# Kernel tuning notes

Hardware: AMD Instinct MI355X
Metric: run time of the kernel (lower is better)

The kernel has to match this reference:

```python
import jax, jax.numpy as jnp
import numpy as np

B, S, D = 64, 14, 2048   # batch, enc_image_size, encoder_dim
A, H, E = 512, 512, 512  # attention_dim, lstm_size, embedding_size
V, L = 10000, 20         # vocab_size, max caption length (T = L-1 decode steps)


def setup_inputs() -> dict:
    key = jax.random.key(0)
    ks = jax.random.split(key, 24)
    p = lambda k, shape: jax.random.normal(k, shape, jnp.float32) * 0.02
    features = jax.random.normal(ks[0], (B, S, S, D), jnp.float32)
    captions = jax.random.randint(ks[1], (B, L), 0, V)
    # sorted descending lengths in [2, L], max forced to L so T_dec = L-1
    lengths = jnp.sort(jax.random.randint(ks[2], (B,), 2, L + 1))[::-1]
    lengths = lengths.at[0].set(L)
    return {
        'features': features, 'captions': captions, 'lengths': lengths,
        'emb': p(ks[3], (V, E)),
        'W_ih': p(ks[4], (4 * H, D + E)), 'b_ih': p(ks[5], (4 * H,)),
        'W_hh': p(ks[6], (4 * H, H)), 'b_hh': p(ks[7], (4 * H,)),
        'h_fc_w': p(ks[8], (H, D)), 'h_fc_b': p(ks[9], (H,)),
        'c_fc_w': p(ks[10], (H, D)), 'c_fc_b': p(ks[11], (H,)),
        'f_beta_w': p(ks[12], (D, H)), 'f_beta_b': p(ks[13], (D,)),
        'cls_w': p(ks[14], (V, H)), 'cls_b': p(ks[15], (V,)),
        'enc_w': p(ks[16], (A, D)), 'enc_b': p(ks[17], (A,)),
        'dec_w': p(ks[18], (A, H)), 'dec_b': p(ks[19], (A,)),
        'att_w': p(ks[20], (1, A)), 'att_b': p(ks[21], (1,)),
    }


def reference(features, captions, lengths, emb, W_ih, b_ih, W_hh, b_hh,
              h_fc_w, h_fc_b, c_fc_w, c_fc_b, f_beta_w, f_beta_b,
              cls_w, cls_b, enc_w, enc_b, dec_w, dec_b, att_w, att_b):
    feats = features.reshape(features.shape[0], -1, features.shape[-1])  # (B,P,D)
    emb_seq = emb[captions]                                              # (B,L,E)
    mean_f = feats.mean(axis=1)
    h = mean_f @ h_fc_w.T + h_fc_b
    c = mean_f @ c_fc_w.T + c_fc_b
    dec_len = lengths - 1
    T = captions.shape[1] - 1
    # attention encoder projection is time-invariant: hoist out of the loop
    att1 = jnp.einsum('bpd,ad->bpa', feats, enc_w) + enc_b               # (B,P,A)

    def step(carry, xs):
        h, c = carry
        x_emb, t = xs
        att2 = h @ dec_w.T + dec_b                                       # (B,A)
        e = jnp.einsum('bpa,a->bp', jax.nn.relu(att1 + att2[:, None, :]), att_w[0]) + att_b[0]
        alpha = jax.nn.softmax(e, axis=1)                                # (B,P)
        awe = jnp.einsum('bp,bpd->bd', alpha, feats)
        gate = jax.nn.sigmoid(h @ f_beta_w.T + f_beta_b)
        awe = gate * awe
        x = jnp.concatenate([x_emb, awe], axis=1)                        # (B,E+D)
        gates = x @ W_ih.T + b_ih + h @ W_hh.T + b_hh                    # torch gate order i,f,g,o
        i, f, g, o = jnp.split(gates, 4, axis=1)
        c2 = jax.nn.sigmoid(f) * c + jax.nn.sigmoid(i) * jnp.tanh(g)
        h2 = jax.nn.sigmoid(o) * jnp.tanh(c2)
        y = h2 @ cls_w.T + cls_b                                         # dropout = eval identity
        active = (t < dec_len)[:, None]
        return (h2, c2), (jnp.where(active, y, 0.0), jnp.where(active, alpha, 0.0))

    xs = (jnp.swapaxes(emb_seq[:, :T], 0, 1), jnp.arange(T))
    (_, _), (y_pred, alphas) = jax.lax.scan(step, (h, c), xs)
    return jnp.swapaxes(y_pred, 0, 1), jnp.swapaxes(alphas, 0, 1)
```

## Files before the change

kernel.cpp:

```cpp
#include <hip/hip_runtime.h>
#include <math.h>

typedef __attribute__((ext_vector_type(8))) short bf16x8;
typedef __attribute__((ext_vector_type(8))) unsigned short u16x8;
typedef __attribute__((ext_vector_type(4))) float f32x4;

#define NB 64
#define NP 196
#define ND 2048
#define NA 512
#define NH 512
#define NE 512
#define NV 10000
#define NT 19
#define NROW (NB*NP)
#define NVP 10112
#define MROW 1280
#define PP 200

__device__ __forceinline__ unsigned short f2bu(float f){
    unsigned int u; __builtin_memcpy(&u, &f, 4);
    u = (u + 0x7FFFu + ((u >> 16) & 1u)) >> 16;
    return (unsigned short)u;
}
__device__ __forceinline__ float b2f(unsigned short s){
    unsigned int u = ((unsigned int)s) << 16;
    float f; __builtin_memcpy(&f, &u, 4); return f;
}
__device__ __forceinline__ float sigm(float x){ return 1.f/(1.f + __expf(-x)); }

__device__ __forceinline__ void gll16(const void* g, void* l){
    __builtin_amdgcn_global_load_lds(
        (const __attribute__((address_space(1))) void*)g,
        (__attribute__((address_space(3))) void*)l, 16, 0, 0);
}


__global__ void k_prep(const float4* __restrict__ enc_w, const float4* __restrict__ dec_w,
                       const float4* __restrict__ f_beta_w, const float4* __restrict__ W_ih,
                       const float4* __restrict__ W_hh, const float4* __restrict__ h_fc_w,
                       const float4* __restrict__ c_fc_w, const float4* __restrict__ cls_w,
                       ushort4* __restrict__ encwb, ushort4* __restrict__ whp,
                       ushort4* __restrict__ wgates, ushort4* __restrict__ wembb,
                       ushort4* __restrict__ whc, ushort4* __restrict__ clswb,
                       ushort4* __restrict__ hsb_pad){
    const int n0 = NA*ND/4;
    const int n1 = 2560*512/4;
    const int n2 = 2048*2560/4;
    const int n3 = 2048*512/4;
    const int n4 = 1024*2048/4;
    const int n5 = NVP*NH/4;
    const int n6 = 64*512/4;
    const int total = n0+n1+n2+n3+n4+n5+n6;
    int stride = gridDim.x*blockDim.x;
    for (int i = blockIdx.x*blockDim.x + threadIdx.x; i < total; i += stride){
        int idx = i;
        float4 v; ushort4 o;
        if (idx < n0){
            v = enc_w[idx];
            o.x = f2bu(v.x); o.y = f2bu(v.y); o.z = f2bu(v.z); o.w = f2bu(v.w);
            encwb[idx] = o; continue;
        }
        idx -= n0;
        if (idx < n1){
            v = (idx < 512*512/4) ? dec_w[idx] : f_beta_w[idx - 512*512/4];
            o.x = f2bu(v.x); o.y = f2bu(v.y); o.z = f2bu(v.z); o.w = f2bu(v.w);
            whp[idx] = o; continue;
        }
        idx -= n1;
        if (idx < n2){
            int j = idx / 640, kk4 = idx - j*640;
            v = (kk4 < 512) ? W_ih[(size_t)j*640 + 128 + kk4] : W_hh[(size_t)j*128 + (kk4 - 512)];
            o.x = f2bu(v.x); o.y = f2bu(v.y); o.z = f2bu(v.z); o.w = f2bu(v.w);
            wgates[idx] = o; continue;
        }
        idx -= n2;
        if (idx < n3){
            int j = idx >> 7, kk4 = idx & 127;
            v = W_ih[(size_t)j*640 + kk4];
            o.x = f2bu(v.x); o.y = f2bu(v.y); o.z = f2bu(v.z); o.w = f2bu(v.w);
            wembb[idx] = o; continue;
        }
        idx -= n3;
        if (idx < n4){
            v = (idx < 512*2048/4) ? h_fc_w[idx] : c_fc_w[idx - 512*2048/4];
            o.x = f2bu(v.x); o.y = f2bu(v.y); o.z = f2bu(v.z); o.w = f2bu(v.w);
            whc[idx] = o; continue;
        }
        idx -= n4;
        if (idx < n5){
            if (idx < NV*NH/4){
                v = cls_w[idx];
                o.x = f2bu(v.x); o.y = f2bu(v.y); o.z = f2bu(v.z); o.w = f2bu(v.w);
            } else { o.x = 0; o.y = 0; o.z = 0; o.w = 0; }
            clswb[idx] = o; continue;
        }
        idx -= n5;
        o.x = 0; o.y = 0; o.z = 0; o.w = 0;
        hsb_pad[idx] = o;
    }
}

__global__ void k_tr3(const float* __restrict__ feats,
                      unsigned short* __restrict__ fbf,
                      unsigned short* __restrict__ ftr,
                      float* __restrict__ mp){
    __shared__ unsigned short sm[64][260];
    __shared__ float4 msum[256];
    int dc = blockIdx.x;
    int b  = blockIdx.y;
    int ph = blockIdx.z;
    int tid = threadIdx.x;
    int c4 = tid & 63;
    int rq = tid >> 6;
    int D0 = dc*256;
    float4 acc = {0.f,0.f,0.f,0.f};
    for (int pcl = 0; pcl < 2; pcl++){
        int pc = ph*2 + pcl;
        __syncthreads();
        #pragma unroll
        for (int i = 0; i < 16; i++){
            int rl = rq + 4*i;
            int p = pc*64 + rl;
            float4 v = {0.f,0.f,0.f,0.f};
            if (p < NP) v = *(const float4*)(feats + ((size_t)(b*NP + p))*ND + D0 + c4*4);
            acc.x += v.x; acc.y += v.y; acc.z += v.z; acc.w += v.w;
            ushort4 u4;
            u4.x = f2bu(v.x); u4.y = f2bu(v.y); u4.z = f2bu(v.z); u4.w = f2bu(v.w);
            if (p < NP) *(ushort4*)(fbf + ((size_t)(b*NP + p))*ND + D0 + c4*4) = u4;
            *(ushort4*)&sm[rl][c4*4] = u4;
        }
        __syncthreads();
        int gmax = (pc == 3) ? 1 : 8;
        for (int g = 0; g < gmax; g++){
            u16x8 o;
            #pragma unroll
            for (int k = 0; k < 8; k++) o[k] = sm[g*8 + k][tid];
            *(u16x8*)(ftr + ((size_t)(b*ND + D0 + tid))*PP + pc*64 + g*8) = o;
        }
    }
    msum[tid] = acc;
    __syncthreads();
    if (tid < 64){
        float4 s0 = msum[tid], s1 = msum[tid+64], s2 = msum[tid+128], s3 = msum[tid+192];
        float4 tot = { (s0.x+s1.x)+(s2.x+s3.x), (s0.y+s1.y)+(s2.y+s3.y),
                       (s0.z+s1.z)+(s2.z+s3.z), (s0.w+s1.w)+(s2.w+s3.w) };
        *(float4*)(mp + ((size_t)ph*64 + b)*ND + D0 + tid*4) = tot;
    }
}

__global__ void k_mean2(const float* __restrict__ mp, unsigned short* __restrict__ meanbf){
    int i = blockIdx.x*1024 + threadIdx.x*4;
    float4 a = *(const float4*)(mp + i);
    float4 b = *(const float4*)(mp + 64*ND + i);
    ushort4 o;
    o.x = f2bu((a.x+b.x)*(1.f/196.f)); o.y = f2bu((a.y+b.y)*(1.f/196.f));
    o.z = f2bu((a.z+b.z)*(1.f/196.f)); o.w = f2bu((a.w+b.w)*(1.f/196.f));
    *(ushort4*)(meanbf + i) = o;
}

__global__ void k_embg(const float* __restrict__ emb, const int* __restrict__ captions,
                       unsigned short* __restrict__ embcat){
    int blk = blockIdx.x, tid = threadIdx.x;
    int r = blk*4 + (tid >> 6);
    int cg = tid & 63;
    u16x8 o;
    #pragma unroll
    for (int k = 0; k < 8; k++) o[k] = 0;
    if (r < NT*64){
        int t = r >> 6, b = r & 63;
        int tok = captions[b*20 + t];
        const float* e = emb + (size_t)tok*NE + cg*8;
        float4 v0 = *(const float4*)e;
        float4 v1 = *(const float4*)(e + 4);
        o[0] = f2bu(v0.x); o[1] = f2bu(v0.y); o[2] = f2bu(v0.z); o[3] = f2bu(v0.w);
        o[4] = f2bu(v1.x); o[5] = f2bu(v1.y); o[6] = f2bu(v1.z); o[7] = f2bu(v1.w);
    }
    *(u16x8*)(embcat + (size_t)r*NE + cg*8) = o;
}

__global__ void k_hc0m(const unsigned short* __restrict__ meanbf,
                       const unsigned short* __restrict__ whc,
                       const float* __restrict__ h_fc_b, const float* __restrict__ c_fc_b,
                       unsigned short* __restrict__ hbf, float* __restrict__ cst){
    int tid = threadIdx.x;
    int w = tid >> 6, l = tid & 63;
    int nt = blockIdx.x;
    int row = 16*w + (l & 15);
    int col = nt*16 + (l & 15);
    int kg = (l >> 4) * 8;
    f32x4 acc = {};
    for (int k0 = 0; k0 < ND; k0 += 32){
        bf16x8 af = *(const bf16x8*)(meanbf + (size_t)row*ND + k0 + kg);
        bf16x8 bv = *(const bf16x8*)(whc + (size_t)col*ND + k0 + kg);
        acc = __builtin_amdgcn_mfma_f32_16x16x32_bf16(af, bv, acc, 0, 0, 0);
    }
    int r0 = 16*w + (l >> 4)*4;
    #pragma unroll
    for (int r = 0; r < 4; r++){
        int b = r0 + r;
        if (col < 512) hbf[b*NH + col] = f2bu(acc[r] + h_fc_b[col]);
        else           cst[b*NH + (col - 512)] = acc[r] + c_fc_b[col - 512];
    }
}

template<int K>
__device__ __forceinline__ void gemm128(const unsigned short* __restrict__ A,
                                        const unsigned short* __restrict__ B,
                                        int brow, int bcol, f32x4 acc[4][4]){
    __shared__ unsigned short As[128*32];
    __shared__ unsigned short Bs[128*32];
    int tid = threadIdx.x;
    int w = tid >> 6, l = tid & 63;
    int wr = (w >> 1) * 64, wc = (w & 1) * 64;
    int lr = l & 15, kg = (l >> 4) * 8;
    const unsigned short* ga0 = A + (size_t)(brow + (tid >> 2))*K + (tid & 3)*8;
    const unsigned short* gb0 = B + (size_t)(bcol + (tid >> 2))*K + (tid & 3)*8;
    for (int k0 = 0; k0 < K; k0 += 32){
        __syncthreads();
        gll16(ga0 + k0,                As + w*512);
        gll16(ga0 + (size_t)64*K + k0, As + 2048 + w*512);
        gll16(gb0 + k0,                Bs + w*512);
        gll16(gb0 + (size_t)64*K + k0, Bs + 2048 + w*512);
        __syncthreads();
        bf16x8 af[4], bfr[4];
        #pragma unroll
        for (int mi = 0; mi < 4; mi++)
            af[mi] = *(const bf16x8*)(As + (wr + mi*16 + lr)*32 + kg);
        #pragma unroll
        for (int ni = 0; ni < 4; ni++)
            bfr[ni] = *(const bf16x8*)(Bs + (wc + ni*16 + lr)*32 + kg);
        #pragma unroll
        for (int ni = 0; ni < 4; ni++){
            #pragma unroll
            for (int mi = 0; mi < 4; mi++)
                acc[mi][ni] = __builtin_amdgcn_mfma_f32_16x16x32_bf16(af[mi], bfr[ni], acc[mi][ni], 0, 0, 0);
        }
    }
}

__global__ void k_gemm_att1(const unsigned short* __restrict__ fbf,
                            const unsigned short* __restrict__ encw,
                            const float* __restrict__ enc_b,
                            unsigned short* __restrict__ att1){
    f32x4 acc[4][4] = {};
    int brow = blockIdx.x*128, bcol = blockIdx.y*128;
    gemm128<ND>(fbf, encw, brow, bcol, acc);
    int w = threadIdx.x >> 6, l = threadIdx.x & 63;
    int wr = (w >> 1) * 64, wc = (w & 1) * 64;
    int r0 = brow + wr + (l >> 4)*4;
    int c0 = bcol + wc + (l & 15);
    #pragma unroll
    for (int ni = 0; ni < 4; ni++){
        int col = c0 + ni*16;
        float eb = enc_b[col];
        #pragma unroll
        for (int mi = 0; mi < 4; mi++){
            #pragma unroll
            for (int r = 0; r < 4; r++)
                att1[(size_t)(r0 + mi*16 + r)*NA + col] = f2bu(acc[mi][ni][r] + eb);
        }
    }
}

__global__ void k_gemb(const unsigned short* __restrict__ embcat,
                       const unsigned short* __restrict__ wembb,
                       const float* __restrict__ b_ih, const float* __restrict__ b_hh,
                       float* __restrict__ gemb){
    f32x4 acc[4][4] = {};
    int brow = blockIdx.x*128, bcol = blockIdx.y*128;
    gemm128<NE>(embcat, wembb, brow, bcol, acc);
    int w = threadIdx.x >> 6, l = threadIdx.x & 63;
    int wr = (w >> 1) * 64, wc = (w & 1) * 64;
    int r0 = brow + wr + (l >> 4)*4;
    int c0 = bcol + wc + (l & 15);
    #pragma unroll
    for (int ni = 0; ni < 4; ni++){
        int col = c0 + ni*16;
        float bias = b_ih[col] + b_hh[col];
        #pragma unroll
        for (int mi = 0; mi < 4; mi++){
            #pragma unroll
            for (int r = 0; r < 4; r++)
                gemb[(size_t)(r0 + mi*16 + r)*2048 + col] = acc[mi][ni][r] + bias;
        }
    }
}

__global__ void k_gemm_cls(const unsigned short* __restrict__ hsb,
                           const unsigned short* __restrict__ clsw,
                           const float* __restrict__ cls_b,
                           const int* __restrict__ lengths,
                           float* __restrict__ yout){
    f32x4 acc[4][4] = {};
    int brow = blockIdx.x*128, bcol = blockIdx.y*128;
    gemm128<NH>(hsb, clsw, brow, bcol, acc);
    int w = threadIdx.x >> 6, l = threadIdx.x & 63;
    int wr = (w >> 1) * 64, wc = (w & 1) * 64;
    int r0 = brow + wr + (l >> 4)*4;
    int c0 = bcol + wc + (l & 15);
    #pragma unroll
    for (int ni = 0; ni < 4; ni++){
        int col = c0 + ni*16;
        if (col >= NV) continue;
        float cb = cls_b[col];
        #pragma unroll
        for (int mi = 0; mi < 4; mi++){
            #pragma unroll
            for (int r = 0; r < 4; r++){
                int grow = r0 + mi*16 + r;
                if (grow >= NT*64) continue;
                int t = grow >> 6, bb = grow & 63;
                int active = t < (lengths[bb] - 1);
                yout[((size_t)bb*NT + t)*NV + col] = active ? (acc[mi][ni][r] + cb) : 0.f;
            }
        }
    }
}


__global__ void k_lstm(const float* __restrict__ part, const float* __restrict__ gemb,
                       float* __restrict__ cst, unsigned short* __restrict__ hbf,
                       unsigned short* __restrict__ hsb, int t){
    int idx = blockIdx.x*256 + threadIdx.x;
    int b = idx >> 9, j = idx & 511;
    const float* ge = gemb + ((size_t)(t - 1)*64 + b)*2048;
    float gi = ge[j], gf = ge[512 + j], gg = ge[1024 + j], go = ge[1536 + j];
    #pragma unroll
    for (int s = 0; s < 10; s++){
        const float* pb = part + (size_t)(s*64 + b)*2048;
        gi += pb[j]; gf += pb[512 + j]; gg += pb[1024 + j]; go += pb[1536 + j];
    }
    float c = cst[b*NH + j];
    float c2 = sigm(gf)*c + sigm(gi)*tanhf(gg);
    float h2 = sigm(go)*tanhf(c2);
    cst[b*NH + j] = c2;
    unsigned short u = f2bu(h2);
    hbf[b*NH + j] = u;
    hsb[((size_t)(t - 1)*64 + b)*NH + j] = u;
}

__global__ void k_hproj(const unsigned short* __restrict__ hbf,
                        const unsigned short* __restrict__ whp,
                        const float* __restrict__ dec_b, const float* __restrict__ f_beta_b,
                        float* __restrict__ hp){
    int w = threadIdx.x >> 6, l = threadIdx.x & 63;
    int nt = blockIdx.x;
    int row = 16*w + (l & 15);
    int col = nt*16 + (l & 15);
    int kg = (l >> 4) * 8;
    f32x4 acc = {};
    for (int k0 = 0; k0 < NH; k0 += 32){
        bf16x8 af = *(const bf16x8*)(hbf + row*NH + k0 + kg);
        bf16x8 bv = *(const bf16x8*)(whp + (size_t)col*NH + k0 + kg);
        acc = __builtin_amdgcn_mfma_f32_16x16x32_bf16(af, bv, acc, 0, 0, 0);
    }
    int r0 = 16*w + (l >> 4)*4;
    float bias = (col < 512) ? dec_b[col] : f_beta_b[col - 512];
    #pragma unroll
    for (int r = 0; r < 4; r++)
        hp[(r0 + r)*2560 + col] = acc[r] + bias;
}

__global__ void k_e(const unsigned short* __restrict__ att1,
                    const float* __restrict__ hp,
                    const float* __restrict__ att_w, const float* __restrict__ att_b,
                    float* __restrict__ ews){
    __shared__ float at2[NA];
    __shared__ float aw[NA];
    int b = blockIdx.x >> 2, pc = blockIdx.x & 3;
    int tid = threadIdx.x;
    for (int j = tid; j < NA; j += 256){
        at2[j] = hp[b*2560 + j];
        aw[j]  = att_w[j];
    }
    __syncthreads();
    int pl = tid >> 2, q = tid & 3;
    if (pl < 49){
        int p = pc*49 + pl;
        const unsigned short* arow = att1 + ((size_t)(b*NP + p))*NA + q*128;
        float s = 0.f;
        for (int a0 = 0; a0 < 128; a0 += 8){
            bf16x8 v = *(const bf16x8*)(arow + a0);
            #pragma unroll
            for (int e = 0; e < 8; e++){
                int ai = q*128 + a0 + e;
                float x = b2f((unsigned short)v[e]) + at2[ai];
                s += fmaxf(x, 0.f) * aw[ai];
            }
        }
        s += __shfl_xor(s, 1);
        s += __shfl_xor(s, 2);
        if (q == 0) ews[b*NP + p] = s + att_b[0];
    }
}

__global__ void k_awe(const float* __restrict__ ews, const unsigned short* __restrict__ ftr,
                      const float* __restrict__ hp, const int* __restrict__ lengths,
                      unsigned short* __restrict__ xg, float* __restrict__ alphas, int t){
    __shared__ float al[PP];
    __shared__ float red[256];
    int dc = blockIdx.x;
    int b  = blockIdx.y;
    int tid = threadIdx.x;
    float v = (tid < NP) ? ews[b*NP + tid] : -1e30f;
    red[tid] = v; __syncthreads();
    for (int s = 128; s > 0; s >>= 1){ if (tid < s) red[tid] = fmaxf(red[tid], red[tid+s]); __syncthreads(); }
    float m = red[0]; __syncthreads();
    float ev = (tid < NP) ? __expf(v - m) : 0.f;
    red[tid] = ev; __syncthreads();
    for (int s = 128; s > 0; s >>= 1){ if (tid < s) red[tid] += red[tid+s]; __syncthreads(); }
    float inv = 1.f / red[0];
    if (tid < NP) al[tid] = ev * inv;
    if (tid >= NP && tid < PP) al[tid] = 0.f;
    __syncthreads();
    if (dc == 0 && tid < NP){
        int active = t < (lengths[b] - 1);
        alphas[((size_t)b*NT + t)*NP + tid] = active ? al[tid] : 0.f;
    }
    int d = dc*256 + tid;
    const unsigned short* fr = ftr + ((size_t)(b*ND + d))*PP;
    float a0 = 0.f, a1 = 0.f, a2 = 0.f, a3 = 0.f;
    #pragma unroll
    for (int c = 0; c < 25; c++){
        bf16x8 vv = *(const bf16x8*)(fr + c*8);
        float ss = 0.f;
        #pragma unroll
        for (int j = 0; j < 8; j++) ss += al[c*8 + j] * b2f((unsigned short)vv[j]);
        if ((c & 3) == 0) a0 += ss; else if ((c & 3) == 1) a1 += ss;
        else if ((c & 3) == 2) a2 += ss; else a3 += ss;
    }
    float accv = (a0 + a1) + (a2 + a3);
    float g = sigm(hp[b*2560 + 512 + d]);
    xg[b*2048 + d] = f2bu(g * accv);
}

__global__ void k_gates(const unsigned short* __restrict__ xg,
                        const unsigned short* __restrict__ hbf,
                        const unsigned short* __restrict__ wgates,
                        float* __restrict__ part){
    int nt = blockIdx.x;
    int s  = blockIdx.y;
    int w = threadIdx.x >> 6, l = threadIdx.x & 63;
    int row = 16*w + (l & 15);
    int col = nt*16 + (l & 15);
    int kg = (l >> 4) * 8;
    const unsigned short* arow = (s < 8) ? (xg + row*2048 + s*256)
                                         : (hbf + row*512 + (s - 8)*256);
    const unsigned short* brow = wgates + (size_t)col*2560 + s*256;
    f32x4 acc = {};
    for (int k0 = 0; k0 < 256; k0 += 32){
        bf16x8 af = *(const bf16x8*)(arow + k0 + kg);
        bf16x8 bv = *(const bf16x8*)(brow + k0 + kg);
        acc = __builtin_amdgcn_mfma_f32_16x16x32_bf16(af, bv, acc, 0, 0, 0);
    }
    int r0 = 16*w + (l >> 4)*4;
    #pragma unroll
    for (int r = 0; r < 4; r++)
        part[(size_t)(s*64 + r0 + r)*2048 + col] = acc[r];
}

__global__ void k_lstm_fin(const float* __restrict__ part, const float* __restrict__ gemb,
                           const float* __restrict__ cst, unsigned short* __restrict__ hsb){
    int idx = blockIdx.x*256 + threadIdx.x;
    int b = idx >> 9, j = idx & 511;
    const float* ge = gemb + ((size_t)(NT - 1)*64 + b)*2048;
    float gi = ge[j], gf = ge[512 + j], gg = ge[1024 + j], go = ge[1536 + j];
    #pragma unroll
    for (int s = 0; s < 10; s++){
        const float* pb = part + (size_t)(s*64 + b)*2048;
        gi += pb[j]; gf += pb[512 + j]; gg += pb[1024 + j]; go += pb[1536 + j];
    }
    float c = cst[b*NH + j];
    float c2 = sigm(gf)*c + sigm(gi)*tanhf(gg);
    float h2 = sigm(go)*tanhf(c2);
    hsb[((size_t)(NT - 1)*64 + b)*NH + j] = f2bu(h2);
}


extern "C" void kernel_launch(void* const* d_in, const int* in_sizes, int n_in,
                              void* d_out, int out_size, void* d_ws, size_t ws_size,
                              hipStream_t stream){
    const float* features = (const float*)d_in[0];
    const int*   captions = (const int*)d_in[1];
    const int*   lengths  = (const int*)d_in[2];
    const float* emb      = (const float*)d_in[3];
    const float* W_ih     = (const float*)d_in[4];
    const float* b_ih     = (const float*)d_in[5];
    const float* W_hh     = (const float*)d_in[6];
    const float* b_hh     = (const float*)d_in[7];
    const float* h_fc_w   = (const float*)d_in[8];
    const float* h_fc_b   = (const float*)d_in[9];
    const float* c_fc_w   = (const float*)d_in[10];
    const float* c_fc_b   = (const float*)d_in[11];
    const float* f_beta_w = (const float*)d_in[12];
    const float* f_beta_b = (const float*)d_in[13];
    const float* cls_w    = (const float*)d_in[14];
    const float* cls_b    = (const float*)d_in[15];
    const float* enc_w    = (const float*)d_in[16];
    const float* enc_b    = (const float*)d_in[17];
    const float* dec_w    = (const float*)d_in[18];
    const float* dec_b    = (const float*)d_in[19];
    const float* att_w    = (const float*)d_in[20];
    const float* att_b    = (const float*)d_in[21];

    char* w = (char*)d_ws;
    size_t off = 0;
    auto alloc = [&](size_t bytes)->char*{
        char* p = w + off;
        off += (bytes + 255) & ~(size_t)255;
        return p;
    };
    unsigned short* fbf    = (unsigned short*)alloc((size_t)NROW*ND*2);
    unsigned short* ftr    = (unsigned short*)alloc((size_t)NB*ND*PP*2);
    unsigned short* att1   = (unsigned short*)alloc((size_t)NROW*NA*2);
    unsigned short* encwb  = (unsigned short*)alloc((size_t)NA*ND*2);
    unsigned short* whp    = (unsigned short*)alloc((size_t)2560*NH*2);
    unsigned short* wgates = (unsigned short*)alloc((size_t)2048*2560*2);
    unsigned short* wembb  = (unsigned short*)alloc((size_t)2048*NE*2);
    unsigned short* whc    = (unsigned short*)alloc((size_t)1024*ND*2);
    unsigned short* clswb  = (unsigned short*)alloc((size_t)NVP*NH*2);
    unsigned short* embcat = (unsigned short*)alloc((size_t)MROW*NE*2);
    unsigned short* hsb    = (unsigned short*)alloc((size_t)MROW*NH*2);
    unsigned short* hbf    = (unsigned short*)alloc((size_t)64*NH*2);
    unsigned short* xg     = (unsigned short*)alloc((size_t)64*2048*2);
    unsigned short* meanbf = (unsigned short*)alloc((size_t)64*ND*2);
    float* mp    = (float*)alloc((size_t)2*64*ND*4);
    float* gemb  = (float*)alloc((size_t)MROW*2048*4);
    float* cst   = (float*)alloc((size_t)64*NH*4);
    float* hp    = (float*)alloc((size_t)64*2560*4);
    float* ews   = (float*)alloc((size_t)64*NP*4);
    float* part  = (float*)alloc((size_t)10*64*2048*4);

    float* yout = (float*)d_out;
    float* alphas_out = yout + (size_t)NB*NT*NV;

    k_tr3<<<dim3(8, 64, 2), 256, 0, stream>>>(features, fbf, ftr, mp);
    k_prep<<<2048, 256, 0, stream>>>((const float4*)enc_w, (const float4*)dec_w,
                                     (const float4*)f_beta_w, (const float4*)W_ih,
                                     (const float4*)W_hh, (const float4*)h_fc_w,
                                     (const float4*)c_fc_w, (const float4*)cls_w,
                                     (ushort4*)encwb, (ushort4*)whp, (ushort4*)wgates,
                                     (ushort4*)wembb, (ushort4*)whc, (ushort4*)clswb,
                                     (ushort4*)(hsb + (size_t)NT*64*NH));
    k_embg<<<320, 256, 0, stream>>>(emb, captions, embcat);
    k_mean2<<<128, 256, 0, stream>>>(mp, meanbf);
    k_hc0m<<<64, 256, 0, stream>>>(meanbf, whc, h_fc_b, c_fc_b, hbf, cst);
    k_gemm_att1<<<dim3(98, 4), 256, 0, stream>>>(fbf, encwb, enc_b, att1);
    k_gemb<<<dim3(10, 16), 256, 0, stream>>>(embcat, wembb, b_ih, b_hh, gemb);

    for (int t = 0; t < NT; t++){
        if (t > 0)
            k_lstm<<<128, 256, 0, stream>>>(part, gemb, cst, hbf, hsb, t);
        k_hproj<<<160, 256, 0, stream>>>(hbf, whp, dec_b, f_beta_b, hp);
        k_e<<<256, 256, 0, stream>>>(att1, hp, att_w, att_b, ews);
        k_awe<<<dim3(8, 64), 256, 0, stream>>>(ews, ftr, hp, lengths, xg, alphas_out, t);
        k_gates<<<dim3(128, 10), 256, 0, stream>>>(xg, hbf, wgates, part);
    }
    k_lstm_fin<<<128, 256, 0, stream>>>(part, gemb, cst, hsb);
    k_gemm_cls<<<dim3(10, 79), 256, 0, stream>>>(hsb, clswb, cls_b, lengths, yout);
}
```

Baseline: 1.125 ms.

## Fuse attention score and weighted sum kernels, fold W_hh into h projection

Merges the per-step attention-score and softmax/weighted-sum kernels into one kernel per batch row that reads the row-major bf16 features directly, dropping the transposed feature copy and its preprocessing. The W_hh matmul moves into the existing h-projection GEMM (output widened to 4608 columns), so the gates GEMM shrinks to the x-part only and the LSTM cell adds the hh slice. The mean reduction is also finished inside the feature conversion kernel, removing one launch. Fewer launches and less preprocessing traffic per decode step are traded for a much smaller grid in the fused attention kernel (128 blocks), with each block recomputing the scores redundantly across its two column chunks.

```diff
diff --git a/kernel.cpp b/kernel.cpp
--- a/kernel.cpp
+++ b/kernel.cpp
@@ -16,7 +16,7 @@
 #define NROW (NB*NP)
 #define NVP 10112
 #define MROW 1280
-#define PP 200
+#define NHP 4608
 
 __device__ __forceinline__ unsigned short f2bu(float f){
     unsigned int u; __builtin_memcpy(&u, &f, 4);
@@ -45,8 +45,8 @@
                        ushort4* __restrict__ whc, ushort4* __restrict__ clswb,
                        ushort4* __restrict__ hsb_pad){
     const int n0 = NA*ND/4;
-    const int n1 = 2560*512/4;
-    const int n2 = 2048*2560/4;
+    const int n1 = NHP*512/4;
+    const int n2 = 2048*2048/4;
     const int n3 = 2048*512/4;
     const int n4 = 1024*2048/4;
     const int n5 = NVP*NH/4;
@@ -63,14 +63,16 @@
         }
         idx -= n0;
         if (idx < n1){
-            v = (idx < 512*512/4) ? dec_w[idx] : f_beta_w[idx - 512*512/4];
+            if (idx < 512*512/4) v = dec_w[idx];
+            else if (idx < 2560*512/4) v = f_beta_w[idx - 512*512/4];
+            else v = W_hh[idx - 2560*512/4];
             o.x = f2bu(v.x); o.y = f2bu(v.y); o.z = f2bu(v.z); o.w = f2bu(v.w);
             whp[idx] = o; continue;
         }
         idx -= n1;
         if (idx < n2){
-            int j = idx / 640, kk4 = idx - j*640;
-            v = (kk4 < 512) ? W_ih[(size_t)j*640 + 128 + kk4] : W_hh[(size_t)j*128 + (kk4 - 512)];
+            int j = idx >> 9, kk4 = idx & 511;
+            v = W_ih[(size_t)j*640 + 128 + kk4];
             o.x = f2bu(v.x); o.y = f2bu(v.y); o.z = f2bu(v.z); o.w = f2bu(v.w);
             wgates[idx] = o; continue;
         }
@@ -101,43 +103,23 @@
     }
 }
 
-__global__ void k_tr3(const float* __restrict__ feats,
-                      unsigned short* __restrict__ fbf,
-                      unsigned short* __restrict__ ftr,
-                      float* __restrict__ mp){
-    __shared__ unsigned short sm[64][260];
+__global__ void k_cm(const float* __restrict__ feats,
+                     unsigned short* __restrict__ fbf,
+                     unsigned short* __restrict__ meanbf){
     __shared__ float4 msum[256];
     int dc = blockIdx.x;
     int b  = blockIdx.y;
-    int ph = blockIdx.z;
     int tid = threadIdx.x;
     int c4 = tid & 63;
     int rq = tid >> 6;
     int D0 = dc*256;
     float4 acc = {0.f,0.f,0.f,0.f};
-    for (int pcl = 0; pcl < 2; pcl++){
-        int pc = ph*2 + pcl;
-        __syncthreads();
-        #pragma unroll
-        for (int i = 0; i < 16; i++){
-            int rl = rq + 4*i;
-            int p = pc*64 + rl;
-            float4 v = {0.f,0.f,0.f,0.f};
-            if (p < NP) v = *(const float4*)(feats + ((size_t)(b*NP + p))*ND + D0 + c4*4);
-            acc.x += v.x; acc.y += v.y; acc.z += v.z; acc.w += v.w;
-            ushort4 u4;
-            u4.x = f2bu(v.x); u4.y = f2bu(v.y); u4.z = f2bu(v.z); u4.w = f2bu(v.w);
-            if (p < NP) *(ushort4*)(fbf + ((size_t)(b*NP + p))*ND + D0 + c4*4) = u4;
-            *(ushort4*)&sm[rl][c4*4] = u4;
-        }
-        __syncthreads();
-        int gmax = (pc == 3) ? 1 : 8;
-        for (int g = 0; g < gmax; g++){
-            u16x8 o;
-            #pragma unroll
-            for (int k = 0; k < 8; k++) o[k] = sm[g*8 + k][tid];
-            *(u16x8*)(ftr + ((size_t)(b*ND + D0 + tid))*PP + pc*64 + g*8) = o;
-        }
+    for (int p = rq; p < NP; p += 4){
+        float4 v = *(const float4*)(feats + ((size_t)(b*NP + p))*ND + D0 + c4*4);
+        acc.x += v.x; acc.y += v.y; acc.z += v.z; acc.w += v.w;
+        ushort4 u4;
+        u4.x = f2bu(v.x); u4.y = f2bu(v.y); u4.z = f2bu(v.z); u4.w = f2bu(v.w);
+        *(ushort4*)(fbf + ((size_t)(b*NP + p))*ND + D0 + c4*4) = u4;
     }
     msum[tid] = acc;
     __syncthreads();
@@ -145,18 +127,11 @@
         float4 s0 = msum[tid], s1 = msum[tid+64], s2 = msum[tid+128], s3 = msum[tid+192];
         float4 tot = { (s0.x+s1.x)+(s2.x+s3.x), (s0.y+s1.y)+(s2.y+s3.y),
                        (s0.z+s1.z)+(s2.z+s3.z), (s0.w+s1.w)+(s2.w+s3.w) };
-        *(float4*)(mp + ((size_t)ph*64 + b)*ND + D0 + tid*4) = tot;
-    }
-}
-
-__global__ void k_mean2(const float* __restrict__ mp, unsigned short* __restrict__ meanbf){
-    int i = blockIdx.x*1024 + threadIdx.x*4;
-    float4 a = *(const float4*)(mp + i);
-    float4 b = *(const float4*)(mp + 64*ND + i);
-    ushort4 o;
-    o.x = f2bu((a.x+b.x)*(1.f/196.f)); o.y = f2bu((a.y+b.y)*(1.f/196.f));
-    o.z = f2bu((a.z+b.z)*(1.f/196.f)); o.w = f2bu((a.w+b.w)*(1.f/196.f));
-    *(ushort4*)(meanbf + i) = o;
+        ushort4 o;
+        o.x = f2bu(tot.x*(1.f/196.f)); o.y = f2bu(tot.y*(1.f/196.f));
+        o.z = f2bu(tot.z*(1.f/196.f)); o.w = f2bu(tot.w*(1.f/196.f));
+        *(ushort4*)(meanbf + (size_t)b*ND + D0 + tid*4) = o;
+    }
 }
 
 __global__ void k_embg(const float* __restrict__ emb, const int* __restrict__ captions,
@@ -320,14 +295,19 @@
 
 
 __global__ void k_lstm(const float* __restrict__ part, const float* __restrict__ gemb,
+                       const float* __restrict__ hp,
                        float* __restrict__ cst, unsigned short* __restrict__ hbf,
                        unsigned short* __restrict__ hsb, int t){
     int idx = blockIdx.x*256 + threadIdx.x;
     int b = idx >> 9, j = idx & 511;
     const float* ge = gemb + ((size_t)(t - 1)*64 + b)*2048;
-    float gi = ge[j], gf = ge[512 + j], gg = ge[1024 + j], go = ge[1536 + j];
-    #pragma unroll
-    for (int s = 0; s < 10; s++){
+    const float* hh = hp + (size_t)b*NHP + 2560;
+    float gi = ge[j]        + hh[j];
+    float gf = ge[512 + j]  + hh[512 + j];
+    float gg = ge[1024 + j] + hh[1024 + j];
+    float go = ge[1536 + j] + hh[1536 + j];
+    #pragma unroll
+    for (int s = 0; s < 8; s++){
         const float* pb = part + (size_t)(s*64 + b)*2048;
         gi += pb[j]; gf += pb[512 + j]; gg += pb[1024 + j]; go += pb[1536 + j];
     }
@@ -340,10 +320,10 @@
     hsb[((size_t)(t - 1)*64 + b)*NH + j] = u;
 }
 
-__global__ void k_hproj(const unsigned short* __restrict__ hbf,
-                        const unsigned short* __restrict__ whp,
-                        const float* __restrict__ dec_b, const float* __restrict__ f_beta_b,
-                        float* __restrict__ hp){
+__global__ void k_hall(const unsigned short* __restrict__ hbf,
+                       const unsigned short* __restrict__ whp,
+                       const float* __restrict__ dec_b, const float* __restrict__ f_beta_b,
+                       float* __restrict__ hp){
     int w = threadIdx.x >> 6, l = threadIdx.x & 63;
     int nt = blockIdx.x;
     int row = 16*w + (l & 15);
@@ -356,87 +336,77 @@
         acc = __builtin_amdgcn_mfma_f32_16x16x32_bf16(af, bv, acc, 0, 0, 0);
     }
     int r0 = 16*w + (l >> 4)*4;
-    float bias = (col < 512) ? dec_b[col] : f_beta_b[col - 512];
+    float bias = (col < 512) ? dec_b[col] : ((col < 2560) ? f_beta_b[col - 512] : 0.f);
     #pragma unroll
     for (int r = 0; r < 4; r++)
-        hp[(r0 + r)*2560 + col] = acc[r] + bias;
-}
-
-__global__ void k_e(const unsigned short* __restrict__ att1,
-                    const float* __restrict__ hp,
-                    const float* __restrict__ att_w, const float* __restrict__ att_b,
-                    float* __restrict__ ews){
+        hp[(size_t)(r0 + r)*NHP + col] = acc[r] + bias;
+}
+
+__global__ void k_eawe(const unsigned short* __restrict__ att1,
+                       const float* __restrict__ hp,
+                       const unsigned short* __restrict__ fbf,
+                       const float* __restrict__ att_w, const float* __restrict__ att_b,
+                       const int* __restrict__ lengths,
+                       unsigned short* __restrict__ xg, float* __restrict__ alphas, int t){
     __shared__ float at2[NA];
     __shared__ float aw[NA];
-    int b = blockIdx.x >> 2, pc = blockIdx.x & 3;
-    int tid = threadIdx.x;
-    for (int j = tid; j < NA; j += 256){
-        at2[j] = hp[b*2560 + j];
-        aw[j]  = att_w[j];
-    }
-    __syncthreads();
-    int pl = tid >> 2, q = tid & 3;
-    if (pl < 49){
-        int p = pc*49 + pl;
-        const unsigned short* arow = att1 + ((size_t)(b*NP + p))*NA + q*128;
-        float s = 0.f;
-        for (int a0 = 0; a0 < 128; a0 += 8){
-            bf16x8 v = *(const bf16x8*)(arow + a0);
-            #pragma unroll
-            for (int e = 0; e < 8; e++){
-                int ai = q*128 + a0 + e;
-                float x = b2f((unsigned short)v[e]) + at2[ai];
-                s += fmaxf(x, 0.f) * aw[ai];
-            }
-        }
-        s += __shfl_xor(s, 1);
-        s += __shfl_xor(s, 2);
-        if (q == 0) ews[b*NP + p] = s + att_b[0];
-    }
-}
-
-__global__ void k_awe(const float* __restrict__ ews, const unsigned short* __restrict__ ftr,
-                      const float* __restrict__ hp, const int* __restrict__ lengths,
-                      unsigned short* __restrict__ xg, float* __restrict__ alphas, int t){
-    __shared__ float al[PP];
+    __shared__ float al[NP];
     __shared__ float red[256];
     int dc = blockIdx.x;
     int b  = blockIdx.y;
     int tid = threadIdx.x;
-    float v = (tid < NP) ? ews[b*NP + tid] : -1e30f;
-    red[tid] = v; __syncthreads();
-    for (int s = 128; s > 0; s >>= 1){ if (tid < s) red[tid] = fmaxf(red[tid], red[tid+s]); __syncthreads(); }
+    for (int j = tid; j < NA; j += 256){
+        at2[j] = hp[(size_t)b*NHP + j];
+        aw[j]  = att_w[j];
+    }
+    __syncthreads();
+    float s = -1e30f;
+    if (tid < NP){
+        const unsigned short* arow = att1 + ((size_t)(b*NP + tid))*NA;
+        float c0 = 0.f, c1 = 0.f, c2 = 0.f, c3 = 0.f;
+        for (int a0 = 0; a0 < 512; a0 += 8){
+            bf16x8 v = *(const bf16x8*)(arow + a0);
+            #pragma unroll
+            for (int e = 0; e < 8; e++){
+                float x = b2f((unsigned short)v[e]) + at2[a0 + e];
+                float m = fmaxf(x, 0.f) * aw[a0 + e];
+                if ((e & 3) == 0) c0 += m; else if ((e & 3) == 1) c1 += m;
+                else if ((e & 3) == 2) c2 += m; else c3 += m;
+            }
+        }
+        s = att_b[0] + (c0 + c1) + (c2 + c3);
+    }
+    red[tid] = s; __syncthreads();
+    for (int st = 128; st > 0; st >>= 1){ if (tid < st) red[tid] = fmaxf(red[tid], red[tid+st]); __syncthreads(); }
     float m = red[0]; __syncthreads();
-    float ev = (tid < NP) ? __expf(v - m) : 0.f;
+    float ev = (tid < NP) ? __expf(s - m) : 0.f;
     red[tid] = ev; __syncthreads();
-    for (int s = 128; s > 0; s >>= 1){ if (tid < s) red[tid] += red[tid+s]; __syncthreads(); }
+    for (int st = 128; st > 0; st >>= 1){ if (tid < st) red[tid] += red[tid+st]; __syncthreads(); }
     float inv = 1.f / red[0];
     if (tid < NP) al[tid] = ev * inv;
-    if (tid >= NP && tid < PP) al[tid] = 0.f;
     __syncthreads();
     if (dc == 0 && tid < NP){
         int active = t < (lengths[b] - 1);
         alphas[((size_t)b*NT + t)*NP + tid] = active ? al[tid] : 0.f;
     }
-    int d = dc*256 + tid;
-    const unsigned short* fr = ftr + ((size_t)(b*ND + d))*PP;
+    int d = dc*1024 + tid*4;
+    const unsigned short* fb = fbf + (size_t)(b*NP)*ND + d;
     float a0 = 0.f, a1 = 0.f, a2 = 0.f, a3 = 0.f;
-    #pragma unroll
-    for (int c = 0; c < 25; c++){
-        bf16x8 vv = *(const bf16x8*)(fr + c*8);
-        float ss = 0.f;
-        #pragma unroll
-        for (int j = 0; j < 8; j++) ss += al[c*8 + j] * b2f((unsigned short)vv[j]);
-        if ((c & 3) == 0) a0 += ss; else if ((c & 3) == 1) a1 += ss;
-        else if ((c & 3) == 2) a2 += ss; else a3 += ss;
-    }
-    float accv = (a0 + a1) + (a2 + a3);
-    float g = sigm(hp[b*2560 + 512 + d]);
-    xg[b*2048 + d] = f2bu(g * accv);
+    #pragma unroll 4
+    for (int p = 0; p < NP; p++){
+        ushort4 v = *(const ushort4*)(fb + (size_t)p*ND);
+        float ap = al[p];
+        a0 += ap * b2f(v.x); a1 += ap * b2f(v.y);
+        a2 += ap * b2f(v.z); a3 += ap * b2f(v.w);
+    }
+    float4 hb = *(const float4*)(hp + (size_t)b*NHP + 512 + d);
+    ushort4 o;
+    o.x = f2bu(sigm(hb.x) * a0); o.y = f2bu(sigm(hb.y) * a1);
+    o.z = f2bu(sigm(hb.z) * a2); o.w = f2bu(sigm(hb.w) * a3);
+    *(ushort4*)(xg + b*2048 + d) = o;
 }
 
 __global__ void k_gates(const unsigned short* __restrict__ xg,
-                        const unsigned short* __restrict__ hbf,
                         const unsigned short* __restrict__ wgates,
                         float* __restrict__ part){
     int nt = blockIdx.x;
@@ -445,9 +415,8 @@
     int row = 16*w + (l & 15);
     int col = nt*16 + (l & 15);
     int kg = (l >> 4) * 8;
-    const unsigned short* arow = (s < 8) ? (xg + row*2048 + s*256)
-                                         : (hbf + row*512 + (s - 8)*256);
-    const unsigned short* brow = wgates + (size_t)col*2560 + s*256;
+    const unsigned short* arow = xg + row*2048 + s*256;
+    const unsigned short* brow = wgates + (size_t)col*2048 + s*256;
     f32x4 acc = {};
     for (int k0 = 0; k0 < 256; k0 += 32){
         bf16x8 af = *(const bf16x8*)(arow + k0 + kg);
@@ -461,13 +430,18 @@
 }
 
 __global__ void k_lstm_fin(const float* __restrict__ part, const float* __restrict__ gemb,
+                           const float* __restrict__ hp,
                            const float* __restrict__ cst, unsigned short* __restrict__ hsb){
     int idx = blockIdx.x*256 + threadIdx.x;
     int b = idx >> 9, j = idx & 511;
     const float* ge = gemb + ((size_t)(NT - 1)*64 + b)*2048;
-    float gi = ge[j], gf = ge[512 + j], gg = ge[1024 + j], go = ge[1536 + j];
-    #pragma unroll
-    for (int s = 0; s < 10; s++){
+    const float* hh = hp + (size_t)b*NHP + 2560;
+    float gi = ge[j]        + hh[j];
+    float gf = ge[512 + j]  + hh[512 + j];
+    float gg = ge[1024 + j] + hh[1024 + j];
+    float go = ge[1536 + j] + hh[1536 + j];
+    #pragma unroll
+    for (int s = 0; s < 8; s++){
         const float* pb = part + (size_t)(s*64 + b)*2048;
         gi += pb[j]; gf += pb[512 + j]; gg += pb[1024 + j]; go += pb[1536 + j];
     }
@@ -512,11 +486,10 @@
         return p;
     };
     unsigned short* fbf    = (unsigned short*)alloc((size_t)NROW*ND*2);
-    unsigned short* ftr    = (unsigned short*)alloc((size_t)NB*ND*PP*2);
     unsigned short* att1   = (unsigned short*)alloc((size_t)NROW*NA*2);
     unsigned short* encwb  = (unsigned short*)alloc((size_t)NA*ND*2);
-    unsigned short* whp    = (unsigned short*)alloc((size_t)2560*NH*2);
-    unsigned short* wgates = (unsigned short*)alloc((size_t)2048*2560*2);
+    unsigned short* whp    = (unsigned short*)alloc((size_t)NHP*NH*2);
+    unsigned short* wgates = (unsigned short*)alloc((size_t)2048*2048*2);
     unsigned short* wembb  = (unsigned short*)alloc((size_t)2048*NE*2);
     unsigned short* whc    = (unsigned short*)alloc((size_t)1024*ND*2);
     unsigned short* clswb  = (unsigned short*)alloc((size_t)NVP*NH*2);
@@ -525,17 +498,15 @@
     unsigned short* hbf    = (unsigned short*)alloc((size_t)64*NH*2);
     unsigned short* xg     = (unsigned short*)alloc((size_t)64*2048*2);
     unsigned short* meanbf = (unsigned short*)alloc((size_t)64*ND*2);
-    float* mp    = (float*)alloc((size_t)2*64*ND*4);
     float* gemb  = (float*)alloc((size_t)MROW*2048*4);
     float* cst   = (float*)alloc((size_t)64*NH*4);
-    float* hp    = (float*)alloc((size_t)64*2560*4);
-    float* ews   = (float*)alloc((size_t)64*NP*4);
-    float* part  = (float*)alloc((size_t)10*64*2048*4);
+    float* hp    = (float*)alloc((size_t)64*NHP*4);
+    float* part  = (float*)alloc((size_t)8*64*2048*4);
 
     float* yout = (float*)d_out;
     float* alphas_out = yout + (size_t)NB*NT*NV;
 
-    k_tr3<<<dim3(8, 64, 2), 256, 0, stream>>>(features, fbf, ftr, mp);
+    k_cm<<<dim3(8, 64), 256, 0, stream>>>(features, fbf, meanbf);
     k_prep<<<2048, 256, 0, stream>>>((const float4*)enc_w, (const float4*)dec_w,
                                      (const float4*)f_beta_w, (const float4*)W_ih,
                                      (const float4*)W_hh, (const float4*)h_fc_w,
@@ -544,19 +515,18 @@
                                      (ushort4*)wembb, (ushort4*)whc, (ushort4*)clswb,
                                      (ushort4*)(hsb + (size_t)NT*64*NH));
     k_embg<<<320, 256, 0, stream>>>(emb, captions, embcat);
-    k_mean2<<<128, 256, 0, stream>>>(mp, meanbf);
     k_hc0m<<<64, 256, 0, stream>>>(meanbf, whc, h_fc_b, c_fc_b, hbf, cst);
     k_gemm_att1<<<dim3(98, 4), 256, 0, stream>>>(fbf, encwb, enc_b, att1);
     k_gemb<<<dim3(10, 16), 256, 0, stream>>>(embcat, wembb, b_ih, b_hh, gemb);
 
     for (int t = 0; t < NT; t++){
         if (t > 0)
-            k_lstm<<<128, 256, 0, stream>>>(part, gemb, cst, hbf, hsb, t);
-        k_hproj<<<160, 256, 0, stream>>>(hbf, whp, dec_b, f_beta_b, hp);
-        k_e<<<256, 256, 0, stream>>>(att1, hp, att_w, att_b, ews);
-        k_awe<<<dim3(8, 64), 256, 0, stream>>>(ews, ftr, hp, lengths, xg, alphas_out, t);
-        k_gates<<<dim3(128, 10), 256, 0, stream>>>(xg, hbf, wgates, part);
-    }
-    k_lstm_fin<<<128, 256, 0, stream>>>(part, gemb, cst, hsb);
+            k_lstm<<<128, 256, 0, stream>>>(part, gemb, hp, cst, hbf, hsb, t);
+        k_hall<<<288, 256, 0, stream>>>(hbf, whp, dec_b, f_beta_b, hp);
+        k_eawe<<<dim3(2, 64), 256, 0, stream>>>(att1, hp, fbf, att_w, att_b,
+                                                lengths, xg, alphas_out, t);
+        k_gates<<<dim3(128, 8), 256, 0, stream>>>(xg, wgates, part);
+    }
+    k_lstm_fin<<<128, 256, 0, stream>>>(part, gemb, hp, cst, hsb);
     k_gemm_cls<<<dim3(10, 79), 256, 0, stream>>>(hsb, clswb, cls_b, lengths, yout);
 }
```

Result: slower. 1.252 ms (+11.3%).
